# Performance work log

Measured on AMD Instinct MI355X. Metric: run time of the kernel, lower is better.

Reference implementation:

```python
import jax, jax.numpy as jnp
import numpy as np

N_NODES = 100000
EPS = 1e-5  # BatchNorm1d default eps


def gcn_conv(x, W, b, row, col, n):
    """PyG GCNConv: add self-loops, symmetric normalization, linear, scatter-add."""
    loop = jnp.arange(n, dtype=row.dtype)
    row_f = jnp.concatenate([row, loop])  # sources
    col_f = jnp.concatenate([col, loop])  # targets
    # degree of target nodes (edge_weight = 1)
    deg = jax.ops.segment_sum(jnp.ones_like(col_f, dtype=x.dtype), col_f, num_segments=n)
    dinv = jnp.where(deg > 0, jax.lax.rsqrt(deg), 0.0)
    norm = dinv[row_f] * dinv[col_f]  # [E+N]
    h = x @ W  # [N, out]
    msg = h[row_f] * norm[:, None]  # [E+N, out]
    out = jax.ops.segment_sum(msg, col_f, num_segments=n)
    return out + b


def batch_norm(x, gamma, beta):
    # training-mode BatchNorm1d: biased batch stats over node axis
    mean = jnp.mean(x, axis=0)
    var = jnp.var(x, axis=0)
    return (x - mean) * jax.lax.rsqrt(var + EPS) * gamma + beta


def setup_inputs() -> dict:
    key = jax.random.key(0)
    ks = jax.random.split(key, 8)
    n, e, f_in, h = N_NODES, 1600000, 25, 128
    x = jax.random.normal(ks[0], (n, f_in), dtype=jnp.float32)
    edge_index = jax.random.randint(ks[1], (2, e), 0, n, dtype=jnp.int64)
    s1 = 1.0 / np.sqrt(f_in)
    s2 = 1.0 / np.sqrt(h)
    W1 = jax.random.uniform(ks[2], (f_in, h), jnp.float32, -s1, s1)
    b1 = jax.random.uniform(ks[3], (h,), jnp.float32, -s1, s1)
    gamma = jnp.ones((h,), jnp.float32)
    beta = jnp.zeros((h,), jnp.float32)
    W2 = jax.random.uniform(ks[4], (h, h), jnp.float32, -s2, s2)
    b2 = jax.random.uniform(ks[5], (h,), jnp.float32, -s2, s2)
    return {"x": x, "edge_index": edge_index, "W1": W1, "b1": b1,
            "gamma": gamma, "beta": beta, "W2": W2, "b2": b2}


def reference(x, edge_index, W1, b1, gamma, beta, W2, b2):
    row, col = edge_index[0], edge_index[1]
    n = x.shape[0]
    h = jax.nn.relu(gcn_conv(x, W1, b1, row, col, n))
    h = batch_norm(h, gamma, beta)
    h = jax.nn.relu(gcn_conv(h, W2, b2, row, col, n))
    return h
```

## Files before the change

kernel.cpp:

```cpp
#include <hip/hip_runtime.h>
#include <stdint.h>


#define HID 128
#define NBB 512

typedef short bf16x8 __attribute__((ext_vector_type(8)));
typedef float f32x4 __attribute__((ext_vector_type(4)));

__device__ __forceinline__ unsigned short f2bf(float f) {
    unsigned int u = __float_as_uint(f);
    unsigned int r = (u + 0x7FFFu + ((u >> 16) & 1u)) >> 16;
    return (unsigned short)r;
}
__device__ __forceinline__ unsigned int pack2bf(float lo, float hi) {
    return (unsigned int)f2bf(lo) | ((unsigned int)f2bf(hi) << 16);
}
__device__ __forceinline__ float bflo(unsigned int v) { return __uint_as_float(v << 16); }
__device__ __forceinline__ float bfhi(unsigned int v) { return __uint_as_float(v & 0xffff0000u); }

__global__ void detect_kernel(const unsigned int* __restrict__ w, int* __restrict__ mode, int nwords) {
    __shared__ int any;
    if (threadIdx.x == 0) any = 0;
    __syncthreads();
    for (int i = threadIdx.x * 2 + 1; i < nwords && i < 8192; i += 512) {
        if (w[i] != 0) atomicOr(&any, 1);
    }
    __syncthreads();
    if (threadIdx.x == 0) *mode = any ? 0 : 1;
}

__device__ __forceinline__ int load_idx(const void* ei, size_t i, int mode) {
    return mode ? (int)((const long long*)ei)[i] : ((const int*)ei)[i];
}

__global__ __launch_bounds__(256) void count_q_kernel(const void* __restrict__ ei,
                                                      const int* __restrict__ modep,
                                                      int* __restrict__ qcnt,
                                                      int E, int CHUNK, int nchunk) {
    __shared__ int qc[512];
    for (int i = threadIdx.x; i < nchunk; i += 256) qc[i] = 0;
    __syncthreads();
    int mode = *modep;
    int beg = blockIdx.x * CHUNK;
    int end = beg + CHUNK; if (end > E) end = E;
    for (int e = beg + threadIdx.x; e < end; e += 256) {
        int c = load_idx(ei, (size_t)E + e, mode);
        atomicAdd(&qc[c >> 8], 1);
    }
    __syncthreads();
    for (int i = threadIdx.x; i < nchunk; i += 256)
        qcnt[blockIdx.x * nchunk + i] = qc[i];
}

__global__ __launch_bounds__(256) void scanq_partial_kernel(const int* __restrict__ qcnt,
                                                            int* __restrict__ blocksum,
                                                            int NQ, int nchunk) {
    int j0 = blockIdx.x * 2048 + threadIdx.x * 8;
    int s = 0;
    #pragma unroll
    for (int i = 0; i < 8; ++i) {
        int j = j0 + i;
        if (j < NQ) {
            int q = j >> 9, b = j & (NBB - 1);
            s += qcnt[b * nchunk + q];
        }
    }
    #pragma unroll
    for (int off = 32; off > 0; off >>= 1) s += __shfl_down(s, off);
    __shared__ int ls[4];
    if ((threadIdx.x & 63) == 0) ls[threadIdx.x >> 6] = s;
    __syncthreads();
    if (threadIdx.x == 0) blocksum[blockIdx.x] = ls[0] + ls[1] + ls[2] + ls[3];
}

__global__ __launch_bounds__(1024) void scanq_blocksums_kernel(const int* __restrict__ blocksum,
                                                               int* __restrict__ blockoff,
                                                               int* __restrict__ qoff,
                                                               int nsb, int NQ) {
    __shared__ int s[1024];
    int t = threadIdx.x;
    int own = (t < nsb) ? blocksum[t] : 0;
    s[t] = own;
    __syncthreads();
    for (int off = 1; off < 1024; off <<= 1) {
        int v = s[t] + ((t >= off) ? s[t - off] : 0);
        __syncthreads();
        s[t] = v;
        __syncthreads();
    }
    if (t < nsb) blockoff[t] = s[t] - own;
    if (t == 1023) qoff[NQ] = s[1023];
}

__global__ __launch_bounds__(256) void scanq_finalize_kernel(const int* __restrict__ qcnt,
                                                             const int* __restrict__ blockoff,
                                                             int* __restrict__ qoff,
                                                             int NQ, int nchunk) {
    int t = threadIdx.x;
    int j0 = blockIdx.x * 2048 + t * 8;
    int v[8], own = 0;
    #pragma unroll
    for (int i = 0; i < 8; ++i) {
        int j = j0 + i;
        v[i] = 0;
        if (j < NQ) {
            int q = j >> 9, b = j & (NBB - 1);
            v[i] = qcnt[b * nchunk + q];
        }
        own += v[i];
    }
    __shared__ int s[256];
    s[t] = own;
    __syncthreads();
    for (int off = 1; off < 256; off <<= 1) {
        int x = s[t] + ((t >= off) ? s[t - off] : 0);
        __syncthreads();
        s[t] = x;
        __syncthreads();
    }
    int e = blockoff[blockIdx.x] + s[t] - own;
    #pragma unroll
    for (int i = 0; i < 8; ++i) {
        int j = j0 + i;
        if (j < NQ) qoff[j] = e;
        e += v[i];
    }
}

__global__ __launch_bounds__(256) void bin_kernel(const void* __restrict__ ei,
                                                  const int* __restrict__ modep,
                                                  const int* __restrict__ qoff,
                                                  unsigned int* __restrict__ packed,
                                                  int E, int CHUNK, int nchunk) {
    __shared__ int cur[512];
    for (int i = threadIdx.x; i < nchunk; i += 256)
        cur[i] = qoff[i * NBB + blockIdx.x];
    __syncthreads();
    int mode = *modep;
    int beg = blockIdx.x * CHUNK;
    int end = beg + CHUNK; if (end > E) end = E;
    for (int e = beg + threadIdx.x; e < end; e += 256) {
        int c = load_idx(ei, (size_t)E + e, mode);
        int r = load_idx(ei, (size_t)e, mode);
        int pos = atomicAdd(&cur[c >> 8], 1);
        packed[pos] = ((unsigned)(c & 255) << 24) | (unsigned)r;
    }
}

__global__ __launch_bounds__(256) void chunk_build_kernel(
    const unsigned int* __restrict__ packed, const int* __restrict__ qoff,
    int* __restrict__ rowptr, float* __restrict__ dinv,
    int* __restrict__ edge_src, int n, int E) {
    int q = blockIdx.x;
    int t = threadIdx.x;
    int pbeg = qoff[q * NBB];
    int pend = qoff[(q + 1) * NBB];
    __shared__ int cnt256[256], cur[256], s[256];
    cnt256[t] = 0;
    __syncthreads();
    for (int i = pbeg + t; i < pend; i += 256)
        atomicAdd(&cnt256[packed[i] >> 24], 1);
    __syncthreads();
    int own = cnt256[t];
    s[t] = own;
    __syncthreads();
    for (int off = 1; off < 256; off <<= 1) {
        int x = s[t] + ((t >= off) ? s[t - off] : 0);
        __syncthreads();
        s[t] = x;
        __syncthreads();
    }
    int pref = s[t] - own;
    int node = (q << 8) + t;
    if (node < n) {
        rowptr[node] = pbeg + pref;
        dinv[node] = rsqrtf((float)(own + 1));
    }
    cur[t] = pbeg + pref;
    if (q == gridDim.x - 1 && t == 0) rowptr[n] = E;
    __syncthreads();
    for (int i = pbeg + t; i < pend; i += 256) {
        unsigned int u = packed[i];
        int pos = atomicAdd(&cur[u >> 24], 1);
        edge_src[pos] = (int)(u & 0xFFFFFFu);
    }
}

__global__ __launch_bounds__(256) void xpad_kernel(const float* __restrict__ x,
                                                   unsigned int* __restrict__ xp, int n) {
    int r = blockIdx.x * 256 + threadIdx.x;
    if (r >= n) return;
    const float* xr = x + (size_t)r * 25;
    unsigned int* o = xp + (size_t)r * 16;
    #pragma unroll
    for (int j = 0; j < 12; ++j)
        o[j] = pack2bf(xr[j * 2], xr[j * 2 + 1]);
    o[12] = pack2bf(xr[24], 0.f);
    o[13] = 0u; o[14] = 0u; o[15] = 0u;
}

__global__ __launch_bounds__(256) void prop_x_kernel(
    const unsigned int* __restrict__ xp, const int* __restrict__ rowptr,
    const int* __restrict__ edge_src, const float* __restrict__ dinv,
    unsigned int* __restrict__ y0, int n) {
    int wid = (blockIdx.x * 256 + threadIdx.x) >> 6;
    if (wid >= n) return;
    int lane = threadIdx.x & 63;
    int g = lane >> 4, i = lane & 15;
    int beg = rowptr[wid], end = rowptr[wid + 1];
    float dc = dinv[wid];
    float ax = 0.f, ay = 0.f;
    for (int b = beg; b < end; b += 64) {
        int m = end - b; if (m > 64) m = 64;
        int s = 0; float w = 0.f;
        if (lane < m) { s = edge_src[b + lane]; w = dinv[s]; }
        int nsteps = (m + 3) >> 2;
        for (int t = 0; t < nsteps; ++t) {
            int e = 4 * t + g;
            int sj = __shfl(s, e & 63);
            float wj = __shfl(w, e & 63);
            if (e >= m) { sj = 0; wj = 0.f; }
            unsigned int u = xp[(size_t)sj * 16 + i];
            ax = fmaf(bflo(u), wj, ax);
            ay = fmaf(bfhi(u), wj, ay);
        }
    }
    if (g == 0) {
        unsigned int u = xp[(size_t)wid * 16 + i];
        ax = fmaf(bflo(u), dc, ax);
        ay = fmaf(bfhi(u), dc, ay);
    }
    ax += __shfl_xor(ax, 16); ax += __shfl_xor(ax, 32);
    ay += __shfl_xor(ay, 16); ay += __shfl_xor(ay, 32);
    if (lane < 16)
        y0[(size_t)wid * 16 + i] = pack2bf(ax * dc, ay * dc);
}

__global__ __launch_bounds__(256) void gemm1_kernel(const unsigned int* __restrict__ y0,
                                                    const float* __restrict__ W,
                                                    const float* __restrict__ bias,
                                                    float* __restrict__ y1, int n) {
    __shared__ float lw[25 * HID];
    for (int i = threadIdx.x; i < 25 * HID; i += 256) lw[i] = W[i];
    __syncthreads();
    int g = threadIdx.x >> 7, c = threadIdx.x & 127;
    float bc = bias[c];
    for (int r = blockIdx.x * 2 + g; r < n; r += gridDim.x * 2) {
        const unsigned int* yr = y0 + (size_t)r * 16;
        float acc = bc;
        #pragma unroll
        for (int j = 0; j < 12; ++j) {
            unsigned int u = yr[j];
            acc = fmaf(bflo(u), lw[(j * 2 + 0) * HID + c], acc);
            acc = fmaf(bfhi(u), lw[(j * 2 + 1) * HID + c], acc);
        }
        acc = fmaf(bflo(yr[12]), lw[24 * HID + c], acc);
        y1[(size_t)r * HID + c] = fmaxf(acc, 0.f);
    }
}

__global__ __launch_bounds__(256) void propagate_kernel(
    const unsigned short* __restrict__ h, const int* __restrict__ rowptr,
    const int* __restrict__ edge_src, const float* __restrict__ dinv,
    const float* __restrict__ bias, float* __restrict__ out, int n) {
    int wid = (blockIdx.x * 256 + threadIdx.x) >> 6;
    if (wid >= n) return;
    int lane = threadIdx.x & 63;
    int beg = rowptr[wid], end = rowptr[wid + 1];
    float dc = dinv[wid];
    float ax = 0.f, ay = 0.f;
    const unsigned int* hp = (const unsigned int*)h;
    for (int b = beg; b < end; b += 64) {
        int m = end - b; if (m > 64) m = 64;
        int s = 0; float w = 0.f;
        if (lane < m) { s = edge_src[b + lane]; w = dinv[s]; }
        int j = 0;
        for (; j + 8 <= m; j += 8) {
            int s0 = __shfl(s, j + 0), s1 = __shfl(s, j + 1);
            int s2 = __shfl(s, j + 2), s3 = __shfl(s, j + 3);
            int s4 = __shfl(s, j + 4), s5 = __shfl(s, j + 5);
            int s6 = __shfl(s, j + 6), s7 = __shfl(s, j + 7);
            unsigned int v0 = hp[(size_t)s0 * 64 + lane];
            unsigned int v1 = hp[(size_t)s1 * 64 + lane];
            unsigned int v2 = hp[(size_t)s2 * 64 + lane];
            unsigned int v3 = hp[(size_t)s3 * 64 + lane];
            unsigned int v4 = hp[(size_t)s4 * 64 + lane];
            unsigned int v5 = hp[(size_t)s5 * 64 + lane];
            unsigned int v6 = hp[(size_t)s6 * 64 + lane];
            unsigned int v7 = hp[(size_t)s7 * 64 + lane];
            float w0 = __shfl(w, j + 0), w1 = __shfl(w, j + 1);
            float w2 = __shfl(w, j + 2), w3 = __shfl(w, j + 3);
            float w4 = __shfl(w, j + 4), w5 = __shfl(w, j + 5);
            float w6 = __shfl(w, j + 6), w7 = __shfl(w, j + 7);
            ax = fmaf(bflo(v0), w0, ax); ay = fmaf(bfhi(v0), w0, ay);
            ax = fmaf(bflo(v1), w1, ax); ay = fmaf(bfhi(v1), w1, ay);
            ax = fmaf(bflo(v2), w2, ax); ay = fmaf(bfhi(v2), w2, ay);
            ax = fmaf(bflo(v3), w3, ax); ay = fmaf(bfhi(v3), w3, ay);
            ax = fmaf(bflo(v4), w4, ax); ay = fmaf(bfhi(v4), w4, ay);
            ax = fmaf(bflo(v5), w5, ax); ay = fmaf(bfhi(v5), w5, ay);
            ax = fmaf(bflo(v6), w6, ax); ay = fmaf(bfhi(v6), w6, ay);
            ax = fmaf(bflo(v7), w7, ax); ay = fmaf(bfhi(v7), w7, ay);
        }
        for (; j < m; ++j) {
            int sj = __shfl(s, j);
            float wj = __shfl(w, j);
            unsigned int v = hp[(size_t)sj * 64 + lane];
            ax = fmaf(bflo(v), wj, ax);
            ay = fmaf(bfhi(v), wj, ay);
        }
    }
    {
        unsigned int v = hp[(size_t)wid * 64 + lane];
        ax = fmaf(bflo(v), dc, ax);
        ay = fmaf(bfhi(v), dc, ay);
    }
    float bx = bias[lane * 2], by = bias[lane * 2 + 1];
    ax = fmaxf(fmaf(ax, dc, bx), 0.f);
    ay = fmaxf(fmaf(ay, dc, by), 0.f);
    *(float2*)(out + (size_t)wid * HID + lane * 2) = make_float2(ax, ay);
}

__global__ __launch_bounds__(256) void bn_stats_kernel(const float* __restrict__ y,
                                                       float* __restrict__ sum,
                                                       float* __restrict__ sumsq, int n) {
    int c = threadIdx.x & 127;
    int g = threadIdx.x >> 7;
    float s = 0.f, s2 = 0.f;
    for (int r = blockIdx.x * 2 + g; r < n; r += gridDim.x * 2) {
        float v = y[(size_t)r * HID + c];
        s += v;
        s2 = fmaf(v, v, s2);
    }
    __shared__ float ls[256], ls2[256];
    ls[threadIdx.x] = s; ls2[threadIdx.x] = s2;
    __syncthreads();
    if (threadIdx.x < 128) {
        atomicAdd(&sum[c], ls[threadIdx.x] + ls[threadIdx.x + 128]);
        atomicAdd(&sumsq[c], ls2[threadIdx.x] + ls2[threadIdx.x + 128]);
    }
}

__global__ void bn_finalize_kernel(const float* __restrict__ sum, const float* __restrict__ sumsq,
                                   const float* __restrict__ gamma, const float* __restrict__ beta,
                                   float* __restrict__ scale, float* __restrict__ shift, float inv_n) {
    int c = threadIdx.x;
    float mean = sum[c] * inv_n;
    float var = sumsq[c] * inv_n - mean * mean;
    float sc = gamma[c] * rsqrtf(var + 1e-5f);
    scale[c] = sc;
    shift[c] = beta[c] - mean * sc;
}

__global__ __launch_bounds__(256) void wt_kernel(const float* __restrict__ W,
                                                 unsigned short* __restrict__ Wt) {
    int idx = blockIdx.x * 256 + threadIdx.x;
    int c = idx >> 7, k = idx & 127;
    Wt[c * 128 + k] = f2bf(W[k * 128 + c]);
}

__global__ __launch_bounds__(256) void gemm2_mfma_kernel(
    const float* __restrict__ y, const unsigned short* __restrict__ Wt,
    const float* __restrict__ scale, const float* __restrict__ shift,
    unsigned short* __restrict__ out, int n) {
    __shared__ unsigned short lwt[128 * 136];
    __shared__ unsigned short ly[128 * 136];
    int t = threadIdx.x;
    int base = blockIdx.x * 128;

    {
        const unsigned int* w32 = (const unsigned int*)Wt;
        unsigned int* l32 = (unsigned int*)lwt;
        #pragma unroll
        for (int i = 0; i < 32; ++i) {
            int idx = t + i * 256;
            int r = idx >> 6, cp = idx & 63;
            l32[r * 68 + cp] = w32[r * 64 + cp];
        }
    }
    {
        int r = t >> 1, hh = t & 1;
        int gr = base + r;
        unsigned int* l32 = (unsigned int*)ly;
        const float4* yrow = (const float4*)(y + (size_t)gr * HID + hh * 64);
        #pragma unroll
        for (int j = 0; j < 16; ++j) {
            float4 v = make_float4(0.f, 0.f, 0.f, 0.f);
            if (gr < n) v = yrow[j];
            int gk = hh * 64 + j * 4;
            float a0 = fmaf(v.x, scale[gk + 0], shift[gk + 0]);
            float a1 = fmaf(v.y, scale[gk + 1], shift[gk + 1]);
            float a2 = fmaf(v.z, scale[gk + 2], shift[gk + 2]);
            float a3 = fmaf(v.w, scale[gk + 3], shift[gk + 3]);
            l32[r * 68 + hh * 32 + j * 2 + 0] = pack2bf(a0, a1);
            l32[r * 68 + hh * 32 + j * 2 + 1] = pack2bf(a2, a3);
        }
    }
    __syncthreads();

    int w = t >> 6, lane = t & 63;
    int li = lane & 15, lg = lane >> 4;
    f32x4 acc[2][8];
    #pragma unroll
    for (int a = 0; a < 2; ++a)
        #pragma unroll
        for (int b = 0; b < 8; ++b) acc[a][b] = (f32x4){0.f, 0.f, 0.f, 0.f};

    #pragma unroll
    for (int ks = 0; ks < 4; ++ks) {
        int kb = ks * 32 + lg * 8;
        bf16x8 af[2], bfr[8];
        #pragma unroll
        for (int rt = 0; rt < 2; ++rt)
            af[rt] = *(const bf16x8*)&ly[(w * 32 + rt * 16 + li) * 136 + kb];
        #pragma unroll
        for (int cf = 0; cf < 8; ++cf)
            bfr[cf] = *(const bf16x8*)&lwt[(cf * 16 + li) * 136 + kb];
        #pragma unroll
        for (int rt = 0; rt < 2; ++rt)
            #pragma unroll
            for (int cf = 0; cf < 8; ++cf)
                acc[rt][cf] = __builtin_amdgcn_mfma_f32_16x16x32_bf16(
                    af[rt], bfr[cf], acc[rt][cf], 0, 0, 0);
    }

    #pragma unroll
    for (int rt = 0; rt < 2; ++rt) {
        #pragma unroll
        for (int reg = 0; reg < 4; ++reg) {
            int gr = base + w * 32 + rt * 16 + lg * 4 + reg;
            if (gr < n) {
                #pragma unroll
                for (int cf = 0; cf < 8; ++cf)
                    out[(size_t)gr * HID + cf * 16 + li] = f2bf(acc[rt][cf][reg]);
            }
        }
    }
}

extern "C" void kernel_launch(void* const* d_in, const int* in_sizes, int n_in,
                              void* d_out, int out_size, void* d_ws, size_t ws_size,
                              hipStream_t stream) {
    const float* x     = (const float*)d_in[0];
    const void*  ei    = d_in[1];
    const float* W1    = (const float*)d_in[2];
    const float* b1    = (const float*)d_in[3];
    const float* gamma = (const float*)d_in[4];
    const float* beta  = (const float*)d_in[5];
    const float* W2    = (const float*)d_in[6];
    const float* b2    = (const float*)d_in[7];
    float* out = (float*)d_out;

    const int f_in = 25;
    int n = in_sizes[0] / f_in;
    int E = in_sizes[1] / 2;
    int nchunk = (n + 255) >> 8;
    int NQ = nchunk * NBB;
    int nsb = (NQ + 2047) / 2048;
    int CHUNK = (E + NBB - 1) / NBB;

    char* ws = (char*)d_ws;
    size_t off = 0;
    auto alloc = [&](size_t bytes) -> void* {
        void* p = ws + off;
        off += (bytes + 511) & ~(size_t)511;
        return p;
    };
    int*   rowptr    = (int*)alloc(((size_t)n + 1) * 4);
    float* dinv      = (float*)alloc((size_t)n * 4);
    int*   edge_src  = (int*)alloc((size_t)E * 4);
    unsigned int* packed = (unsigned int*)alloc((size_t)E * 4);
    int*   qcnt      = (int*)alloc((size_t)NQ * 4);
    int*   qoff      = (int*)alloc(((size_t)NQ + 1) * 4);
    int*   blocksum  = (int*)alloc((size_t)nsb * 4);
    int*   blockoff  = (int*)alloc((size_t)nsb * 4);
    float* bnacc     = (float*)alloc(256 * 4);
    float* sclshift  = (float*)alloc(256 * 4);
    int*   mode      = (int*)alloc(4);
    unsigned int* xp  = (unsigned int*)alloc((size_t)n * 16 * 4);
    unsigned int* y0  = (unsigned int*)alloc((size_t)n * 16 * 4);
    unsigned short* Wt = (unsigned short*)alloc(128 * 128 * 2);
    unsigned short* h  = (unsigned short*)alloc((size_t)n * HID * 2);

    hipMemsetAsync(bnacc, 0, 256 * 4, stream);

    detect_kernel<<<1, 256, 0, stream>>>((const unsigned int*)ei, mode, 2 * E);
    count_q_kernel<<<NBB, 256, 0, stream>>>(ei, mode, qcnt, E, CHUNK, nchunk);
    scanq_partial_kernel<<<nsb, 256, 0, stream>>>(qcnt, blocksum, NQ, nchunk);
    scanq_blocksums_kernel<<<1, 1024, 0, stream>>>(blocksum, blockoff, qoff, nsb, NQ);
    scanq_finalize_kernel<<<nsb, 256, 0, stream>>>(qcnt, blockoff, qoff, NQ, nchunk);
    bin_kernel<<<NBB, 256, 0, stream>>>(ei, mode, qoff, packed, E, CHUNK, nchunk);
    chunk_build_kernel<<<nchunk, 256, 0, stream>>>(packed, qoff, rowptr, dinv, edge_src, n, E);

    xpad_kernel<<<(n + 255) / 256, 256, 0, stream>>>(x, xp, n);
    prop_x_kernel<<<(n + 3) / 4, 256, 0, stream>>>(xp, rowptr, edge_src, dinv, y0, n);
    gemm1_kernel<<<4096, 256, 0, stream>>>(y0, W1, b1, out, n);

    bn_stats_kernel<<<512, 256, 0, stream>>>(out, bnacc, bnacc + 128, n);
    bn_finalize_kernel<<<1, 128, 0, stream>>>(bnacc, bnacc + 128, gamma, beta,
                                              sclshift, sclshift + 128, 1.0f / (float)n);

    wt_kernel<<<64, 256, 0, stream>>>(W2, Wt);
    gemm2_mfma_kernel<<<(n + 127) / 128, 256, 0, stream>>>(out, Wt, sclshift, sclshift + 128, h, n);
    propagate_kernel<<<(n + 3) / 4, 256, 0, stream>>>(h, rowptr, edge_src, dinv, b2, out, n);
}
```

Baseline: 282.4 us.

## Fuse BN statistics into gemm1 and widen propagate gathers to two edges per wave

Measured after the change: 278.9 us. No clear change (-1.2%).

```diff
diff --git a/kernel.cpp b/kernel.cpp
--- a/kernel.cpp
+++ b/kernel.cpp
@@ -240,12 +240,15 @@
 __global__ __launch_bounds__(256) void gemm1_kernel(const unsigned int* __restrict__ y0,
                                                     const float* __restrict__ W,
                                                     const float* __restrict__ bias,
-                                                    float* __restrict__ y1, int n) {
+                                                    float* __restrict__ y1,
+                                                    float* __restrict__ bnsum,
+                                                    float* __restrict__ bnsumsq, int n) {
     __shared__ float lw[25 * HID];
     for (int i = threadIdx.x; i < 25 * HID; i += 256) lw[i] = W[i];
     __syncthreads();
     int g = threadIdx.x >> 7, c = threadIdx.x & 127;
     float bc = bias[c];
+    float s = 0.f, s2 = 0.f;
     for (int r = blockIdx.x * 2 + g; r < n; r += gridDim.x * 2) {
         const unsigned int* yr = y0 + (size_t)r * 16;
         float acc = bc;
@@ -256,7 +259,17 @@
             acc = fmaf(bfhi(u), lw[(j * 2 + 1) * HID + c], acc);
         }
         acc = fmaf(bflo(yr[12]), lw[24 * HID + c], acc);
-        y1[(size_t)r * HID + c] = fmaxf(acc, 0.f);
+        acc = fmaxf(acc, 0.f);
+        y1[(size_t)r * HID + c] = acc;
+        s += acc;
+        s2 = fmaf(acc, acc, s2);
+    }
+    __shared__ float ls[256], ls2[256];
+    ls[threadIdx.x] = s; ls2[threadIdx.x] = s2;
+    __syncthreads();
+    if (threadIdx.x < 128) {
+        atomicAdd(&bnsum[c], ls[threadIdx.x] + ls[threadIdx.x + 128]);
+        atomicAdd(&bnsumsq[c], ls2[threadIdx.x] + ls2[threadIdx.x + 128]);
     }
 }
 
@@ -267,77 +280,76 @@
     int wid = (blockIdx.x * 256 + threadIdx.x) >> 6;
     if (wid >= n) return;
     int lane = threadIdx.x & 63;
+    int half = lane >> 5;
+    int f = lane & 31;
     int beg = rowptr[wid], end = rowptr[wid + 1];
     float dc = dinv[wid];
-    float ax = 0.f, ay = 0.f;
-    const unsigned int* hp = (const unsigned int*)h;
+    float a0 = 0.f, a1 = 0.f, a2 = 0.f, a3 = 0.f;
+    const uint2* hp = (const uint2*)h;
     for (int b = beg; b < end; b += 64) {
         int m = end - b; if (m > 64) m = 64;
         int s = 0; float w = 0.f;
         if (lane < m) { s = edge_src[b + lane]; w = dinv[s]; }
         int j = 0;
-        for (; j + 8 <= m; j += 8) {
-            int s0 = __shfl(s, j + 0), s1 = __shfl(s, j + 1);
-            int s2 = __shfl(s, j + 2), s3 = __shfl(s, j + 3);
-            int s4 = __shfl(s, j + 4), s5 = __shfl(s, j + 5);
-            int s6 = __shfl(s, j + 6), s7 = __shfl(s, j + 7);
-            unsigned int v0 = hp[(size_t)s0 * 64 + lane];
-            unsigned int v1 = hp[(size_t)s1 * 64 + lane];
-            unsigned int v2 = hp[(size_t)s2 * 64 + lane];
-            unsigned int v3 = hp[(size_t)s3 * 64 + lane];
-            unsigned int v4 = hp[(size_t)s4 * 64 + lane];
-            unsigned int v5 = hp[(size_t)s5 * 64 + lane];
-            unsigned int v6 = hp[(size_t)s6 * 64 + lane];
-            unsigned int v7 = hp[(size_t)s7 * 64 + lane];
-            float w0 = __shfl(w, j + 0), w1 = __shfl(w, j + 1);
-            float w2 = __shfl(w, j + 2), w3 = __shfl(w, j + 3);
-            float w4 = __shfl(w, j + 4), w5 = __shfl(w, j + 5);
-            float w6 = __shfl(w, j + 6), w7 = __shfl(w, j + 7);
-            ax = fmaf(bflo(v0), w0, ax); ay = fmaf(bfhi(v0), w0, ay);
-            ax = fmaf(bflo(v1), w1, ax); ay = fmaf(bfhi(v1), w1, ay);
-            ax = fmaf(bflo(v2), w2, ax); ay = fmaf(bfhi(v2), w2, ay);
-            ax = fmaf(bflo(v3), w3, ax); ay = fmaf(bfhi(v3), w3, ay);
-            ax = fmaf(bflo(v4), w4, ax); ay = fmaf(bfhi(v4), w4, ay);
-            ax = fmaf(bflo(v5), w5, ax); ay = fmaf(bfhi(v5), w5, ay);
-            ax = fmaf(bflo(v6), w6, ax); ay = fmaf(bfhi(v6), w6, ay);
-            ax = fmaf(bflo(v7), w7, ax); ay = fmaf(bfhi(v7), w7, ay);
-        }
-        for (; j < m; ++j) {
-            int sj = __shfl(s, j);
-            float wj = __shfl(w, j);
-            unsigned int v = hp[(size_t)sj * 64 + lane];
-            ax = fmaf(bflo(v), wj, ax);
-            ay = fmaf(bfhi(v), wj, ay);
-        }
-    }
+        for (; j + 16 <= m; j += 16) {
+            int e0_ = j + half,      e1_ = j + 2 + half,  e2_ = j + 4 + half,  e3_ = j + 6 + half;
+            int e4_ = j + 8 + half,  e5_ = j + 10 + half, e6_ = j + 12 + half, e7_ = j + 14 + half;
+            int t0 = __shfl(s, e0_), t1 = __shfl(s, e1_), t2 = __shfl(s, e2_), t3 = __shfl(s, e3_);
+            int t4 = __shfl(s, e4_), t5 = __shfl(s, e5_), t6 = __shfl(s, e6_), t7 = __shfl(s, e7_);
+            uint2 v0 = hp[(size_t)t0 * 32 + f];
+            uint2 v1 = hp[(size_t)t1 * 32 + f];
+            uint2 v2 = hp[(size_t)t2 * 32 + f];
+            uint2 v3 = hp[(size_t)t3 * 32 + f];
+            uint2 v4 = hp[(size_t)t4 * 32 + f];
+            uint2 v5 = hp[(size_t)t5 * 32 + f];
+            uint2 v6 = hp[(size_t)t6 * 32 + f];
+            uint2 v7 = hp[(size_t)t7 * 32 + f];
+            float w0 = __shfl(w, e0_), w1 = __shfl(w, e1_), w2 = __shfl(w, e2_), w3 = __shfl(w, e3_);
+            float w4 = __shfl(w, e4_), w5 = __shfl(w, e5_), w6 = __shfl(w, e6_), w7 = __shfl(w, e7_);
+            a0 = fmaf(bflo(v0.x), w0, a0); a1 = fmaf(bfhi(v0.x), w0, a1);
+            a2 = fmaf(bflo(v0.y), w0, a2); a3 = fmaf(bfhi(v0.y), w0, a3);
+            a0 = fmaf(bflo(v1.x), w1, a0); a1 = fmaf(bfhi(v1.x), w1, a1);
+            a2 = fmaf(bflo(v1.y), w1, a2); a3 = fmaf(bfhi(v1.y), w1, a3);
+            a0 = fmaf(bflo(v2.x), w2, a0); a1 = fmaf(bfhi(v2.x), w2, a1);
+            a2 = fmaf(bflo(v2.y), w2, a2); a3 = fmaf(bfhi(v2.y), w2, a3);
+            a0 = fmaf(bflo(v3.x), w3, a0); a1 = fmaf(bfhi(v3.x), w3, a1);
+            a2 = fmaf(bflo(v3.y), w3, a2); a3 = fmaf(bfhi(v3.y), w3, a3);
+            a0 = fmaf(bflo(v4.x), w4, a0); a1 = fmaf(bfhi(v4.x), w4, a1);
+            a2 = fmaf(bflo(v4.y), w4, a2); a3 = fmaf(bfhi(v4.y), w4, a3);
+            a0 = fmaf(bflo(v5.x), w5, a0); a1 = fmaf(bfhi(v5.x), w5, a1);
+            a2 = fmaf(bflo(v5.y), w5, a2); a3 = fmaf(bfhi(v5.y), w5, a3);
+            a0 = fmaf(bflo(v6.x), w6, a0); a1 = fmaf(bfhi(v6.x), w6, a1);
+            a2 = fmaf(bflo(v6.y), w6, a2); a3 = fmaf(bfhi(v6.y), w6, a3);
+            a0 = fmaf(bflo(v7.x), w7, a0); a1 = fmaf(bfhi(v7.x), w7, a1);
+            a2 = fmaf(bflo(v7.y), w7, a2); a3 = fmaf(bfhi(v7.y), w7, a3);
+        }
+        for (; j < m; j += 2) {
+            int e = j + half;
+            int sj = __shfl(s, e & 63);
+            float wj = __shfl(w, e & 63);
+            if (e >= m) { sj = 0; wj = 0.f; }
+            uint2 v = hp[(size_t)sj * 32 + f];
+            a0 = fmaf(bflo(v.x), wj, a0); a1 = fmaf(bfhi(v.x), wj, a1);
+            a2 = fmaf(bflo(v.y), wj, a2); a3 = fmaf(bfhi(v.y), wj, a3);
+        }
+    }
+    a0 += __shfl_xor(a0, 32);
+    a1 += __shfl_xor(a1, 32);
+    a2 += __shfl_xor(a2, 32);
+    a3 += __shfl_xor(a3, 32);
     {
-        unsigned int v = hp[(size_t)wid * 64 + lane];
-        ax = fmaf(bflo(v), dc, ax);
-        ay = fmaf(bfhi(v), dc, ay);
-    }
-    float bx = bias[lane * 2], by = bias[lane * 2 + 1];
-    ax = fmaxf(fmaf(ax, dc, bx), 0.f);
-    ay = fmaxf(fmaf(ay, dc, by), 0.f);
-    *(float2*)(out + (size_t)wid * HID + lane * 2) = make_float2(ax, ay);
-}
-
-__global__ __launch_bounds__(256) void bn_stats_kernel(const float* __restrict__ y,
-                                                       float* __restrict__ sum,
-                                                       float* __restrict__ sumsq, int n) {
-    int c = threadIdx.x & 127;
-    int g = threadIdx.x >> 7;
-    float s = 0.f, s2 = 0.f;
-    for (int r = blockIdx.x * 2 + g; r < n; r += gridDim.x * 2) {
-        float v = y[(size_t)r * HID + c];
-        s += v;
-        s2 = fmaf(v, v, s2);
-    }
-    __shared__ float ls[256], ls2[256];
-    ls[threadIdx.x] = s; ls2[threadIdx.x] = s2;
-    __syncthreads();
-    if (threadIdx.x < 128) {
-        atomicAdd(&sum[c], ls[threadIdx.x] + ls[threadIdx.x + 128]);
-        atomicAdd(&sumsq[c], ls2[threadIdx.x] + ls2[threadIdx.x + 128]);
+        uint2 v = hp[(size_t)wid * 32 + f];
+        a0 = fmaf(bflo(v.x), dc, a0); a1 = fmaf(bfhi(v.x), dc, a1);
+        a2 = fmaf(bflo(v.y), dc, a2); a3 = fmaf(bfhi(v.y), dc, a3);
+    }
+    if (lane < 32) {
+        float4 bv = ((const float4*)bias)[f];
+        float4 r;
+        r.x = fmaxf(fmaf(a0, dc, bv.x), 0.f);
+        r.y = fmaxf(fmaf(a1, dc, bv.y), 0.f);
+        r.z = fmaxf(fmaf(a2, dc, bv.z), 0.f);
+        r.w = fmaxf(fmaf(a3, dc, bv.w), 0.f);
+        *(float4*)(out + (size_t)wid * HID + f * 4) = r;
     }
 }
 
@@ -494,9 +506,8 @@
 
     xpad_kernel<<<(n + 255) / 256, 256, 0, stream>>>(x, xp, n);
     prop_x_kernel<<<(n + 3) / 4, 256, 0, stream>>>(xp, rowptr, edge_src, dinv, y0, n);
-    gemm1_kernel<<<4096, 256, 0, stream>>>(y0, W1, b1, out, n);
-
-    bn_stats_kernel<<<512, 256, 0, stream>>>(out, bnacc, bnacc + 128, n);
+    gemm1_kernel<<<1024, 256, 0, stream>>>(y0, W1, b1, out, bnacc, bnacc + 128, n);
+
     bn_finalize_kernel<<<1, 128, 0, stream>>>(bnacc, bnacc + 128, gamma, beta,
                                               sclshift, sclshift + 128, 1.0f / (float)n);
 
```
